# Kernel optimization log

Hardware: AMD Instinct MI355X
Metric: run time of the kernel (lower is better)

The kernel has to match this reference:

```python
import jax, jax.numpy as jnp
import numpy as np

B, N, D = 2, 256, 512
H = 4 * D  # mlp_hidden_dim


def setup_inputs() -> dict:
    key = jax.random.key(0)
    ks = jax.random.split(key, 14)
    s_in = 1.0 / np.sqrt(D)
    s_h = 1.0 / np.sqrt(H)
    s_cat = 1.0 / np.sqrt(2 * D)
    return {
        "x_v": jax.random.normal(ks[0], (B, N, D), jnp.float32),
        "x_a": jax.random.normal(ks[1], (B, N, D), jnp.float32),
        # weights stored as (in, out); y = x @ W + b (same math as torch Linear)
        "W1v": jax.random.uniform(ks[2], (D, H), jnp.float32, -s_in, s_in),
        "b1v": jax.random.uniform(ks[3], (H,), jnp.float32, -s_in, s_in),
        "W1a": jax.random.uniform(ks[4], (D, H), jnp.float32, -s_in, s_in),
        "b1a": jax.random.uniform(ks[5], (H,), jnp.float32, -s_in, s_in),
        "Wmv": jax.random.uniform(ks[6], (H, D), jnp.float32, -s_h, s_h),
        "bmv": jax.random.uniform(ks[7], (D,), jnp.float32, -s_h, s_h),
        "Wma": jax.random.uniform(ks[8], (H, D), jnp.float32, -s_h, s_h),
        "bma": jax.random.uniform(ks[9], (D,), jnp.float32, -s_h, s_h),
        "Wout": jax.random.uniform(ks[10], (2 * D, D), jnp.float32, -s_cat, s_cat),
        "bout": jax.random.uniform(ks[11], (D,), jnp.float32, -s_cat, s_cat),
    }


def reference(x_v, x_a, W1v, b1v, W1a, b1a, Wmv, bmv, Wma, bma, Wout, bout):
    # pairwise Manhattan distance: [B, N, M]
    dist = jnp.sum(jnp.abs(x_v[:, :, None, :] - x_a[:, None, :, :]), axis=-1)
    dv = dist.mean(axis=2)  # [B, N] mean distance of each v-token to all a-tokens
    da = dist.mean(axis=1)  # [B, M]
    xv_w = x_v * dv[..., None]
    xa_w = x_a * da[..., None]
    # dropout prob = 0.0 -> identity
    hv = jax.nn.gelu(xv_w @ W1v + b1v, approximate=False) @ Wmv + bmv
    ha = jax.nn.gelu(xa_w @ W1a + b1a, approximate=False) @ Wma + bma
    combined = jnp.concatenate([hv, ha], axis=-1)  # [B, N, 2D]
    return combined @ Wout + bout
```

## Files before the change

kernel.cpp:

```cpp
#include <hip/hip_runtime.h>
#include <math.h>

#define Bsz  2
#define Ntok 256
#define Ddim 512
#define Hdim 2048
#define Mrows (Bsz * Ntok)

typedef __bf16 bf16_8 __attribute__((ext_vector_type(8)));
typedef __bf16 bf16_4 __attribute__((ext_vector_type(4)));
typedef float  f32x4_t __attribute__((ext_vector_type(4)));

struct PrepPtrs {
    const float* src[5];
    __bf16*      dst[5];
    const float* xv;
    const float* xa;
    float*       pv;
    float*       pa;
};

__global__ __launch_bounds__(256) void prep_kernel(PrepPtrs p) {
    __shared__ float tile[32][33];
    __shared__ float red[4][4];

    int blk = blockIdx.x;
    int tid = threadIdx.x;

    if (blk < 4608) {
        const int Ks[5]  = {512, 512, 2048, 2048, 1024};
        const int Ns[5]  = {2048, 2048, 512, 512, 512};
        const int off[6] = {0, 1024, 2048, 3072, 4096, 4608};
        int mi = 0;
        while (blk >= off[mi + 1]) ++mi;
        int local = blk - off[mi];
        int shift = (mi < 2) ? 6 : 4;
        int bx = local & ((1 << shift) - 1);
        int by = local >> shift;
        const float* src = p.src[mi];
        __bf16*      dst = p.dst[mi];
        int K = Ks[mi], N = Ns[mi];
        int n0 = bx << 5, k0 = by << 5;

        int kl = tid >> 3, nl = (tid & 7) << 2;
        float4 v = *(const float4*)&src[(size_t)(k0 + kl) * N + n0 + nl];
        tile[kl][nl + 0] = v.x;
        tile[kl][nl + 1] = v.y;
        tile[kl][nl + 2] = v.z;
        tile[kl][nl + 3] = v.w;
        __syncthreads();
        int nl2 = tid >> 3, kl2 = (tid & 7) << 2;
        bf16_4 o;
#pragma unroll
        for (int i = 0; i < 4; ++i) o[i] = (__bf16)tile[kl2 + i][nl2];
        *(bf16_4*)&dst[(size_t)(n0 + nl2) * K + k0 + kl2] = o;
    } else {
        int bx   = blk - 4608;
        int jc   = bx & 3;
        int g    = bx >> 2;
        int role = g >> 7;
        int b    = (g >> 6) & 1;
        int i0   = (g & 63) << 2;
        const float* Q    = role ? p.xa : p.xv;
        const float* S    = role ? p.xv : p.xa;
        float*       outp = role ? p.pa : p.pv;

        int d0 = tid << 1;
        const float* Qb = Q + ((size_t)b * Ntok + i0) * Ddim + d0;
        const float* Sb = S + ((size_t)b * Ntok + (jc << 6)) * Ddim + d0;

        float2 q[4];
#pragma unroll
        for (int r = 0; r < 4; ++r) q[r] = *(const float2*)(Qb + r * Ddim);

        float acc[4] = {0.f, 0.f, 0.f, 0.f};
#pragma unroll 4
        for (int j = 0; j < 64; ++j) {
            float2 s = *(const float2*)(Sb + (size_t)j * Ddim);
#pragma unroll
            for (int r = 0; r < 4; ++r)
                acc[r] += fabsf(q[r].x - s.x) + fabsf(q[r].y - s.y);
        }
        int lane = tid & 63, wv = tid >> 6;
#pragma unroll
        for (int r = 0; r < 4; ++r) {
            float v = acc[r];
#pragma unroll
            for (int off2 = 32; off2; off2 >>= 1) v += __shfl_down(v, off2);
            if (lane == 0) red[wv][r] = v;
        }
        __syncthreads();
        if (tid < 4) {
            float v = red[0][tid] + red[1][tid] + red[2][tid] + red[3][tid];
            outp[jc * Mrows + b * Ntok + i0 + tid] = v;
        }
    }
}

struct GPtrs {
    const void*   A[2];
    const __bf16* BT[2];
    const float*  bias[2];
    const float*  scale[2];
    void*         C[2];
};

template <int AFP32>
struct StageA {
    float4 f0, f1;
};
template <>
struct StageA<0> {
    bf16_8 a8;
};

template <int GELU, int AFP32, int OUTBF16>
__global__ __launch_bounds__(256) void mfma_gemm(GPtrs p, int Kdim, int ldc) {
    __shared__ __align__(16) __bf16 As[2][64][40];
    __shared__ __align__(16) __bf16 Bs[2][64][40];

    const int zi  = blockIdx.z;
    const int tid = threadIdx.x;
    const int m0 = blockIdx.y << 6, n0 = blockIdx.x << 6;

    const int row = tid >> 2;
    const int kc  = (tid & 3) << 3;

    const __bf16* Bp = p.BT[zi] + (size_t)(n0 + row) * Kdim + kc;
    const float*  Afp = nullptr;
    const __bf16* Abp = nullptr;
    float s = 1.0f;
    if (AFP32) {
        Afp = (const float*)p.A[zi] + (size_t)(m0 + row) * Kdim + kc;
        const float* ps = p.scale[zi];
        int m = m0 + row;
        s = (ps[m] + ps[Mrows + m] + ps[2 * Mrows + m] + ps[3 * Mrows + m])
            * (1.0f / 256.0f);
    } else {
        Abp = (const __bf16*)p.A[zi] + (size_t)(m0 + row) * Kdim + kc;
    }

    const int wave = tid >> 6, lane = tid & 63;
    const int moff = (wave >> 1) << 5, noff = (wave & 1) << 5;
    const int lrow = lane & 15, quad = lane >> 4;

    auto loadStage = [&](int kt, StageA<AFP32>& st, bf16_8& bb) {
        bb = *(const bf16_8*)(Bp + kt);
        if constexpr (AFP32) {
            st.f0 = *(const float4*)(Afp + kt);
            st.f1 = *(const float4*)(Afp + kt + 4);
        } else {
            st.a8 = *(const bf16_8*)(Abp + kt);
        }
    };
    auto storeStage = [&](int buf, const StageA<AFP32>& st, const bf16_8& bb) {
        bf16_8 a8;
        if constexpr (AFP32) {
            a8[0] = (__bf16)(st.f0.x * s); a8[1] = (__bf16)(st.f0.y * s);
            a8[2] = (__bf16)(st.f0.z * s); a8[3] = (__bf16)(st.f0.w * s);
            a8[4] = (__bf16)(st.f1.x * s); a8[5] = (__bf16)(st.f1.y * s);
            a8[6] = (__bf16)(st.f1.z * s); a8[7] = (__bf16)(st.f1.w * s);
        } else {
            a8 = st.a8;
        }
        *(bf16_8*)&As[buf][row][kc] = a8;
        *(bf16_8*)&Bs[buf][row][kc] = bb;
    };

    f32x4_t acc00 = {0.f, 0.f, 0.f, 0.f};
    f32x4_t acc01 = {0.f, 0.f, 0.f, 0.f};
    f32x4_t acc10 = {0.f, 0.f, 0.f, 0.f};
    f32x4_t acc11 = {0.f, 0.f, 0.f, 0.f};

    const int nIter = Kdim >> 5;
    StageA<AFP32> stR, stN;
    bf16_8 bR, bN;

    {
        StageA<AFP32> st0; bf16_8 b0;
        loadStage(0, st0, b0);
        storeStage(0, st0, b0);
    }
    if (nIter > 1) loadStage(32, stR, bR);
    __syncthreads();

    for (int it = 0; it < nIter; ++it) {
        const int cur = it & 1;
        bf16_8 a0 = *(const bf16_8*)&As[cur][moff + lrow][quad << 3];
        bf16_8 a1 = *(const bf16_8*)&As[cur][moff + 16 + lrow][quad << 3];
        bf16_8 b0 = *(const bf16_8*)&Bs[cur][noff + lrow][quad << 3];
        bf16_8 b1 = *(const bf16_8*)&Bs[cur][noff + 16 + lrow][quad << 3];
        if (it + 2 < nIter) loadStage((it + 2) << 5, stN, bN);
        acc00 = __builtin_amdgcn_mfma_f32_16x16x32_bf16(a0, b0, acc00, 0, 0, 0);
        acc01 = __builtin_amdgcn_mfma_f32_16x16x32_bf16(a0, b1, acc01, 0, 0, 0);
        acc10 = __builtin_amdgcn_mfma_f32_16x16x32_bf16(a1, b0, acc10, 0, 0, 0);
        acc11 = __builtin_amdgcn_mfma_f32_16x16x32_bf16(a1, b1, acc11, 0, 0, 0);
        if (it + 1 < nIter) {
            storeStage(cur ^ 1, stR, bR);
            stR = stN; bR = bN;
            __syncthreads();
        }
    }

    const float* bias = p.bias[zi];
    f32x4_t accs[2][2] = {{acc00, acc01}, {acc10, acc11}};
#pragma unroll
    for (int ti = 0; ti < 2; ++ti) {
#pragma unroll
        for (int tj = 0; tj < 2; ++tj) {
            int colg = n0 + noff + (tj << 4) + lrow;
            float bv = bias[colg];
#pragma unroll
            for (int r = 0; r < 4; ++r) {
                int rowg = m0 + moff + (ti << 4) + (quad << 2) + r;
                float v = accs[ti][tj][r] + bv;
                if (GELU) v = 0.5f * v * (1.0f + erff(v * 0.70710678118654752f));
                if (OUTBF16)
                    ((__bf16*)p.C[zi])[(size_t)rowg * ldc + colg] = (__bf16)v;
                else
                    ((float*)p.C[zi])[(size_t)rowg * ldc + colg] = v;
            }
        }
    }
}

extern "C" void kernel_launch(void* const* d_in, const int* in_sizes, int n_in,
                              void* d_out, int out_size, void* d_ws, size_t ws_size,
                              hipStream_t stream) {
    const float* x_v  = (const float*)d_in[0];
    const float* x_a  = (const float*)d_in[1];
    const float* W1v  = (const float*)d_in[2];
    const float* b1v  = (const float*)d_in[3];
    const float* W1a  = (const float*)d_in[4];
    const float* b1a  = (const float*)d_in[5];
    const float* Wmv  = (const float*)d_in[6];
    const float* bmv  = (const float*)d_in[7];
    const float* Wma  = (const float*)d_in[8];
    const float* bma  = (const float*)d_in[9];
    const float* Wout = (const float*)d_in[10];
    const float* bout = (const float*)d_in[11];
    float* out = (float*)d_out;

    char* w = (char*)d_ws;
    auto alloc = [&](size_t bytes) {
        char* r = w;
        w += (bytes + 255) & ~(size_t)255;
        return (void*)r;
    };
    float*  pv    = (float*)alloc(4 * Mrows * 4);
    float*  pa    = (float*)alloc(4 * Mrows * 4);
    __bf16* WT1v  = (__bf16*)alloc((size_t)Hdim * Ddim * 2);
    __bf16* WT1a  = (__bf16*)alloc((size_t)Hdim * Ddim * 2);
    __bf16* WTmv  = (__bf16*)alloc((size_t)Ddim * Hdim * 2);
    __bf16* WTma  = (__bf16*)alloc((size_t)Ddim * Hdim * 2);
    __bf16* WTout = (__bf16*)alloc((size_t)Ddim * 2 * Ddim * 2);
    __bf16* g1v   = (__bf16*)alloc((size_t)Mrows * Hdim * 2);
    __bf16* g1a   = (__bf16*)alloc((size_t)Mrows * Hdim * 2);
    __bf16* comb  = (__bf16*)alloc((size_t)Mrows * 2 * Ddim * 2);

    PrepPtrs pp;
    pp.src[0] = W1v;  pp.dst[0] = WT1v;
    pp.src[1] = W1a;  pp.dst[1] = WT1a;
    pp.src[2] = Wmv;  pp.dst[2] = WTmv;
    pp.src[3] = Wma;  pp.dst[3] = WTma;
    pp.src[4] = Wout; pp.dst[4] = WTout;
    pp.xv = x_v; pp.xa = x_a; pp.pv = pv; pp.pa = pa;
    prep_kernel<<<dim3(5632), dim3(256), 0, stream>>>(pp);

    GPtrs g1;
    g1.A[0] = x_v; g1.A[1] = x_a;
    g1.BT[0] = WT1v; g1.BT[1] = WT1a;
    g1.bias[0] = b1v; g1.bias[1] = b1a;
    g1.scale[0] = pv; g1.scale[1] = pa;
    g1.C[0] = g1v; g1.C[1] = g1a;
    mfma_gemm<1, 1, 1><<<dim3(Hdim / 64, Mrows / 64, 2), dim3(256), 0, stream>>>(
        g1, Ddim, Hdim);

    GPtrs g2;
    g2.A[0] = g1v; g2.A[1] = g1a;
    g2.BT[0] = WTmv; g2.BT[1] = WTma;
    g2.bias[0] = bmv; g2.bias[1] = bma;
    g2.scale[0] = nullptr; g2.scale[1] = nullptr;
    g2.C[0] = comb; g2.C[1] = comb + Ddim;
    mfma_gemm<0, 0, 1><<<dim3(Ddim / 64, Mrows / 64, 2), dim3(256), 0, stream>>>(
        g2, Hdim, 2 * Ddim);

    GPtrs g3;
    g3.A[0] = comb; g3.A[1] = comb;
    g3.BT[0] = WTout; g3.BT[1] = WTout;
    g3.bias[0] = bout; g3.bias[1] = bout;
    g3.scale[0] = nullptr; g3.scale[1] = nullptr;
    g3.C[0] = out; g3.C[1] = out;
    mfma_gemm<0, 0, 0><<<dim3(Ddim / 64, Mrows / 64, 1), dim3(256), 0, stream>>>(
        g3, 2 * Ddim, Ddim);
}
```

Baseline: 151.3 us.

## Fuse three GEMMs into one persistent kernel with grid barriers and split-K

```diff
diff --git a/kernel.cpp b/kernel.cpp
--- a/kernel.cpp
+++ b/kernel.cpp
@@ -5,7 +5,7 @@
 #define Ntok 256
 #define Ddim 512
 #define Hdim 2048
-#define Mrows (Bsz * Ntok)
+#define Mrows 512
 
 typedef __bf16 bf16_8 __attribute__((ext_vector_type(8)));
 typedef __bf16 bf16_4 __attribute__((ext_vector_type(4)));
@@ -18,6 +18,8 @@
     const float* xa;
     float*       pv;
     float*       pa;
+    float*       out;
+    unsigned*    ctr;
 };
 
 __global__ __launch_bounds__(256) void prep_kernel(PrepPtrs p) {
@@ -54,7 +56,7 @@
 #pragma unroll
         for (int i = 0; i < 4; ++i) o[i] = (__bf16)tile[kl2 + i][nl2];
         *(bf16_4*)&dst[(size_t)(n0 + nl2) * K + k0 + kl2] = o;
-    } else {
+    } else if (blk < 5632) {
         int bx   = blk - 4608;
         int jc   = bx & 3;
         int g    = bx >> 2;
@@ -94,77 +96,95 @@
             float v = red[0][tid] + red[1][tid] + red[2][tid] + red[3][tid];
             outp[jc * Mrows + b * Ntok + i0 + tid] = v;
         }
-    }
-}
-
-struct GPtrs {
-    const void*   A[2];
-    const __bf16* BT[2];
-    const float*  bias[2];
-    const float*  scale[2];
-    void*         C[2];
-};
-
-template <int AFP32>
-struct StageA {
-    float4 f0, f1;
-};
-template <>
-struct StageA<0> {
-    bf16_8 a8;
-};
-
-template <int GELU, int AFP32, int OUTBF16>
-__global__ __launch_bounds__(256) void mfma_gemm(GPtrs p, int Kdim, int ldc) {
-    __shared__ __align__(16) __bf16 As[2][64][40];
-    __shared__ __align__(16) __bf16 Bs[2][64][40];
-
-    const int zi  = blockIdx.z;
+    } else {
+        int zb = blk - 5632;
+        float4 z4 = {0.f, 0.f, 0.f, 0.f};
+        *(float4*)&p.out[((size_t)zb * 256 + tid) * 4] = z4;
+        if (zb == 0 && tid == 0) *p.ctr = 0u;
+    }
+}
+
+__device__ __forceinline__ void gbar(unsigned* ctr, unsigned target) {
+    __syncthreads();
+    __threadfence();
+    if (threadIdx.x == 0) {
+        atomicAdd(ctr, 1u);
+        while (atomicAdd(ctr, 0u) < target)
+            __builtin_amdgcn_s_sleep(2);
+    }
+    __syncthreads();
+    __threadfence();
+}
+
+template <int GELU, int AMODE, int OUTM>
+__device__ void gemm_tile(__bf16 (&As)[2][64][40], __bf16 (&Bs)[2][64][40],
+                          const void* Aa, const void* Ab, int lda,
+                          const __bf16* BT, int ldb,
+                          const float* bias, const float* scale4,
+                          void* C, int ldc, int Kdim,
+                          int m0, int n0, int addBias) {
     const int tid = threadIdx.x;
-    const int m0 = blockIdx.y << 6, n0 = blockIdx.x << 6;
-
     const int row = tid >> 2;
     const int kc  = (tid & 3) << 3;
 
-    const __bf16* Bp = p.BT[zi] + (size_t)(n0 + row) * Kdim + kc;
-    const float*  Afp = nullptr;
+    const __bf16* Bp  = BT + (size_t)(n0 + row) * ldb + kc;
+    const float*  Af0 = nullptr;
+    const float*  Af1 = nullptr;
     const __bf16* Abp = nullptr;
     float s = 1.0f;
-    if (AFP32) {
-        Afp = (const float*)p.A[zi] + (size_t)(m0 + row) * Kdim + kc;
-        const float* ps = p.scale[zi];
+    if (AMODE == 1) {
+        Af0 = (const float*)Aa + (size_t)(m0 + row) * lda + kc;
         int m = m0 + row;
-        s = (ps[m] + ps[Mrows + m] + ps[2 * Mrows + m] + ps[3 * Mrows + m])
-            * (1.0f / 256.0f);
+        s = (scale4[m] + scale4[Mrows + m] + scale4[2 * Mrows + m] +
+             scale4[3 * Mrows + m]) * (1.0f / 256.0f);
+    } else if (AMODE == 2) {
+        Af0 = (const float*)Aa + (size_t)(m0 + row) * lda + kc;
+        Af1 = (const float*)Ab + (size_t)(m0 + row) * lda + kc;
     } else {
-        Abp = (const __bf16*)p.A[zi] + (size_t)(m0 + row) * Kdim + kc;
+        Abp = (const __bf16*)Aa + (size_t)(m0 + row) * lda + kc;
     }
 
     const int wave = tid >> 6, lane = tid & 63;
     const int moff = (wave >> 1) << 5, noff = (wave & 1) << 5;
     const int lrow = lane & 15, quad = lane >> 4;
 
-    auto loadStage = [&](int kt, StageA<AFP32>& st, bf16_8& bb) {
-        bb = *(const bf16_8*)(Bp + kt);
-        if constexpr (AFP32) {
-            st.f0 = *(const float4*)(Afp + kt);
-            st.f1 = *(const float4*)(Afp + kt + 4);
+    float4 rA0, rA1, rB0, rB1, nA0, nA1, nB0, nB1;
+    bf16_8 ra8, na8;
+    bf16_8 rb8, nb8;
+
+    auto loadStage = [&](int kt, float4& fa0, float4& fa1, float4& fb0,
+                         float4& fb1, bf16_8& a8, bf16_8& b8) {
+        b8 = *(const bf16_8*)(Bp + kt);
+        if (AMODE == 0) {
+            a8 = *(const bf16_8*)(Abp + kt);
         } else {
-            st.a8 = *(const bf16_8*)(Abp + kt);
+            fa0 = *(const float4*)(Af0 + kt);
+            fa1 = *(const float4*)(Af0 + kt + 4);
+            if (AMODE == 2) {
+                fb0 = *(const float4*)(Af1 + kt);
+                fb1 = *(const float4*)(Af1 + kt + 4);
+            }
         }
     };
-    auto storeStage = [&](int buf, const StageA<AFP32>& st, const bf16_8& bb) {
+    auto storeStage = [&](int buf, const float4& fa0, const float4& fa1,
+                          const float4& fb0, const float4& fb1,
+                          const bf16_8& a8in, const bf16_8& b8in) {
         bf16_8 a8;
-        if constexpr (AFP32) {
-            a8[0] = (__bf16)(st.f0.x * s); a8[1] = (__bf16)(st.f0.y * s);
-            a8[2] = (__bf16)(st.f0.z * s); a8[3] = (__bf16)(st.f0.w * s);
-            a8[4] = (__bf16)(st.f1.x * s); a8[5] = (__bf16)(st.f1.y * s);
-            a8[6] = (__bf16)(st.f1.z * s); a8[7] = (__bf16)(st.f1.w * s);
+        if (AMODE == 0) {
+            a8 = a8in;
+        } else if (AMODE == 1) {
+            a8[0] = (__bf16)(fa0.x * s); a8[1] = (__bf16)(fa0.y * s);
+            a8[2] = (__bf16)(fa0.z * s); a8[3] = (__bf16)(fa0.w * s);
+            a8[4] = (__bf16)(fa1.x * s); a8[5] = (__bf16)(fa1.y * s);
+            a8[6] = (__bf16)(fa1.z * s); a8[7] = (__bf16)(fa1.w * s);
         } else {
-            a8 = st.a8;
+            a8[0] = (__bf16)(fa0.x + fb0.x); a8[1] = (__bf16)(fa0.y + fb0.y);
+            a8[2] = (__bf16)(fa0.z + fb0.z); a8[3] = (__bf16)(fa0.w + fb0.w);
+            a8[4] = (__bf16)(fa1.x + fb1.x); a8[5] = (__bf16)(fa1.y + fb1.y);
+            a8[6] = (__bf16)(fa1.z + fb1.z); a8[7] = (__bf16)(fa1.w + fb1.w);
         }
         *(bf16_8*)&As[buf][row][kc] = a8;
-        *(bf16_8*)&Bs[buf][row][kc] = bb;
+        *(bf16_8*)&Bs[buf][row][kc] = b8in;
     };
 
     f32x4_t acc00 = {0.f, 0.f, 0.f, 0.f};
@@ -173,15 +193,11 @@
     f32x4_t acc11 = {0.f, 0.f, 0.f, 0.f};
 
     const int nIter = Kdim >> 5;
-    StageA<AFP32> stR, stN;
-    bf16_8 bR, bN;
-
-    {
-        StageA<AFP32> st0; bf16_8 b0;
-        loadStage(0, st0, b0);
-        storeStage(0, st0, b0);
-    }
-    if (nIter > 1) loadStage(32, stR, bR);
+
+    __syncthreads();
+    loadStage(0, rA0, rA1, rB0, rB1, ra8, rb8);
+    storeStage(0, rA0, rA1, rB0, rB1, ra8, rb8);
+    if (nIter > 1) loadStage(32, rA0, rA1, rB0, rB1, ra8, rb8);
     __syncthreads();
 
     for (int it = 0; it < nIter; ++it) {
@@ -190,37 +206,86 @@
         bf16_8 a1 = *(const bf16_8*)&As[cur][moff + 16 + lrow][quad << 3];
         bf16_8 b0 = *(const bf16_8*)&Bs[cur][noff + lrow][quad << 3];
         bf16_8 b1 = *(const bf16_8*)&Bs[cur][noff + 16 + lrow][quad << 3];
-        if (it + 2 < nIter) loadStage((it + 2) << 5, stN, bN);
+        if (it + 2 < nIter)
+            loadStage((it + 2) << 5, nA0, nA1, nB0, nB1, na8, nb8);
         acc00 = __builtin_amdgcn_mfma_f32_16x16x32_bf16(a0, b0, acc00, 0, 0, 0);
         acc01 = __builtin_amdgcn_mfma_f32_16x16x32_bf16(a0, b1, acc01, 0, 0, 0);
         acc10 = __builtin_amdgcn_mfma_f32_16x16x32_bf16(a1, b0, acc10, 0, 0, 0);
         acc11 = __builtin_amdgcn_mfma_f32_16x16x32_bf16(a1, b1, acc11, 0, 0, 0);
         if (it + 1 < nIter) {
-            storeStage(cur ^ 1, stR, bR);
-            stR = stN; bR = bN;
+            storeStage(cur ^ 1, rA0, rA1, rB0, rB1, ra8, rb8);
+            rA0 = nA0; rA1 = nA1; rB0 = nB0; rB1 = nB1; ra8 = na8; rb8 = nb8;
             __syncthreads();
         }
     }
 
-    const float* bias = p.bias[zi];
     f32x4_t accs[2][2] = {{acc00, acc01}, {acc10, acc11}};
 #pragma unroll
     for (int ti = 0; ti < 2; ++ti) {
 #pragma unroll
         for (int tj = 0; tj < 2; ++tj) {
             int colg = n0 + noff + (tj << 4) + lrow;
-            float bv = bias[colg];
+            float bv = addBias ? bias[colg] : 0.0f;
 #pragma unroll
             for (int r = 0; r < 4; ++r) {
                 int rowg = m0 + moff + (ti << 4) + (quad << 2) + r;
                 float v = accs[ti][tj][r] + bv;
                 if (GELU) v = 0.5f * v * (1.0f + erff(v * 0.70710678118654752f));
-                if (OUTBF16)
-                    ((__bf16*)p.C[zi])[(size_t)rowg * ldc + colg] = (__bf16)v;
+                if (OUTM == 1)
+                    ((__bf16*)C)[(size_t)rowg * ldc + colg] = (__bf16)v;
+                else if (OUTM == 0)
+                    ((float*)C)[(size_t)rowg * ldc + colg] = v;
                 else
-                    ((float*)p.C[zi])[(size_t)rowg * ldc + colg] = v;
+                    atomicAdd((float*)C + (size_t)rowg * ldc + colg, v);
             }
         }
+    }
+}
+
+struct FPtrs {
+    const float*  x[2];
+    const __bf16* WT1[2];
+    const float*  b1[2];
+    const float*  pd[2];
+    __bf16*       g1[2];
+    const __bf16* WTm[2];
+    const float*  bm[2];
+    float*        part[2];
+    const __bf16* WTout;
+    const float*  bout;
+    float*        out;
+    unsigned*     ctr;
+};
+
+__global__ __launch_bounds__(256) void fused_gemms(FPtrs p) {
+    __shared__ __align__(16) __bf16 As[2][64][40];
+    __shared__ __align__(16) __bf16 Bs[2][64][40];
+    const int blk = blockIdx.x;
+
+    for (int t = blk; t < 512; t += 256) {
+        int z  = t >> 8;
+        int nt = t & 31, mt = (t >> 5) & 7;
+        gemm_tile<1, 1, 1>(As, Bs, p.x[z], nullptr, Ddim, p.WT1[z], Ddim,
+                           p.b1[z], p.pd[z], p.g1[z], Hdim, Ddim,
+                           mt << 6, nt << 6, 1);
+    }
+    gbar(p.ctr, 256);
+
+    {
+        int nt = blk & 7, mt = (blk >> 3) & 7, z = (blk >> 6) & 1, kz = blk >> 7;
+        gemm_tile<0, 0, 0>(As, Bs, p.g1[z] + kz * 1024, nullptr, Hdim,
+                           p.WTm[z] + kz * 1024, Hdim, p.bm[z], nullptr,
+                           p.part[kz] + z * Ddim, 2 * Ddim, 1024,
+                           mt << 6, nt << 6, kz == 0);
+    }
+    gbar(p.ctr, 512);
+
+    {
+        int nt = blk & 7, mt = (blk >> 3) & 7, kz = blk >> 6;
+        gemm_tile<0, 2, 2>(As, Bs, p.part[0] + kz * 256, p.part[1] + kz * 256,
+                           2 * Ddim, p.WTout + kz * 256, 2 * Ddim, p.bout,
+                           nullptr, p.out, Ddim, 256, mt << 6, nt << 6,
+                           kz == 0);
     }
 }
 
@@ -247,16 +312,18 @@
         w += (bytes + 255) & ~(size_t)255;
         return (void*)r;
     };
-    float*  pv    = (float*)alloc(4 * Mrows * 4);
-    float*  pa    = (float*)alloc(4 * Mrows * 4);
-    __bf16* WT1v  = (__bf16*)alloc((size_t)Hdim * Ddim * 2);
-    __bf16* WT1a  = (__bf16*)alloc((size_t)Hdim * Ddim * 2);
-    __bf16* WTmv  = (__bf16*)alloc((size_t)Ddim * Hdim * 2);
-    __bf16* WTma  = (__bf16*)alloc((size_t)Ddim * Hdim * 2);
-    __bf16* WTout = (__bf16*)alloc((size_t)Ddim * 2 * Ddim * 2);
-    __bf16* g1v   = (__bf16*)alloc((size_t)Mrows * Hdim * 2);
-    __bf16* g1a   = (__bf16*)alloc((size_t)Mrows * Hdim * 2);
-    __bf16* comb  = (__bf16*)alloc((size_t)Mrows * 2 * Ddim * 2);
+    float*    pv    = (float*)alloc(4 * Mrows * 4);
+    float*    pa    = (float*)alloc(4 * Mrows * 4);
+    unsigned* ctr   = (unsigned*)alloc(256);
+    __bf16*   WT1v  = (__bf16*)alloc((size_t)Hdim * Ddim * 2);
+    __bf16*   WT1a  = (__bf16*)alloc((size_t)Hdim * Ddim * 2);
+    __bf16*   WTmv  = (__bf16*)alloc((size_t)Ddim * Hdim * 2);
+    __bf16*   WTma  = (__bf16*)alloc((size_t)Ddim * Hdim * 2);
+    __bf16*   WTout = (__bf16*)alloc((size_t)Ddim * 2 * Ddim * 2);
+    __bf16*   g1v   = (__bf16*)alloc((size_t)Mrows * Hdim * 2);
+    __bf16*   g1a   = (__bf16*)alloc((size_t)Mrows * Hdim * 2);
+    float*    part0 = (float*)alloc((size_t)Mrows * 2 * Ddim * 4);
+    float*    part1 = (float*)alloc((size_t)Mrows * 2 * Ddim * 4);
 
     PrepPtrs pp;
     pp.src[0] = W1v;  pp.dst[0] = WT1v;
@@ -265,32 +332,19 @@
     pp.src[3] = Wma;  pp.dst[3] = WTma;
     pp.src[4] = Wout; pp.dst[4] = WTout;
     pp.xv = x_v; pp.xa = x_a; pp.pv = pv; pp.pa = pa;
-    prep_kernel<<<dim3(5632), dim3(256), 0, stream>>>(pp);
-
-    GPtrs g1;
-    g1.A[0] = x_v; g1.A[1] = x_a;
-    g1.BT[0] = WT1v; g1.BT[1] = WT1a;
-    g1.bias[0] = b1v; g1.bias[1] = b1a;
-    g1.scale[0] = pv; g1.scale[1] = pa;
-    g1.C[0] = g1v; g1.C[1] = g1a;
-    mfma_gemm<1, 1, 1><<<dim3(Hdim / 64, Mrows / 64, 2), dim3(256), 0, stream>>>(
-        g1, Ddim, Hdim);
-
-    GPtrs g2;
-    g2.A[0] = g1v; g2.A[1] = g1a;
-    g2.BT[0] = WTmv; g2.BT[1] = WTma;
-    g2.bias[0] = bmv; g2.bias[1] = bma;
-    g2.scale[0] = nullptr; g2.scale[1] = nullptr;
-    g2.C[0] = comb; g2.C[1] = comb + Ddim;
-    mfma_gemm<0, 0, 1><<<dim3(Ddim / 64, Mrows / 64, 2), dim3(256), 0, stream>>>(
-        g2, Hdim, 2 * Ddim);
-
-    GPtrs g3;
-    g3.A[0] = comb; g3.A[1] = comb;
-    g3.BT[0] = WTout; g3.BT[1] = WTout;
-    g3.bias[0] = bout; g3.bias[1] = bout;
-    g3.scale[0] = nullptr; g3.scale[1] = nullptr;
-    g3.C[0] = out; g3.C[1] = out;
-    mfma_gemm<0, 0, 0><<<dim3(Ddim / 64, Mrows / 64, 1), dim3(256), 0, stream>>>(
-        g3, 2 * Ddim, Ddim);
-}
+    pp.out = out; pp.ctr = ctr;
+    prep_kernel<<<dim3(5888), dim3(256), 0, stream>>>(pp);
+
+    FPtrs fp;
+    fp.x[0] = x_v; fp.x[1] = x_a;
+    fp.WT1[0] = WT1v; fp.WT1[1] = WT1a;
+    fp.b1[0] = b1v; fp.b1[1] = b1a;
+    fp.pd[0] = pv; fp.pd[1] = pa;
+    fp.g1[0] = g1v; fp.g1[1] = g1a;
+    fp.WTm[0] = WTmv; fp.WTm[1] = WTma;
+    fp.bm[0] = bmv; fp.bm[1] = bma;
+    fp.part[0] = part0; fp.part[1] = part1;
+    fp.WTout = WTout; fp.bout = bout;
+    fp.out = out; fp.ctr = ctr;
+    fused_gemms<<<dim3(256), dim3(256), 0, stream>>>(fp);
+}
```

New measurement: 230.5 us. 1.52x slower.
